# Kernel tuning notes

Hardware: AMD Instinct MI355X
Metric: run time of the kernel (lower is better)

## Reference

```python
import jax, jax.numpy as jnp
import numpy as np

ITER = 50
SMOOTH = 1e-05


def _max_pool(x, window):
    # x: [B, C, D, H, W]; 'same' max pool with stride 1, -inf padding
    # (matches torch F.max_pool3d semantics with symmetric padding).
    win = (1, 1) + window
    pads = [(0, 0), (0, 0)] + [((w - 1) // 2, (w - 1) // 2) for w in window]
    return jax.lax.reduce_window(x, -jnp.inf, jax.lax.max, win, (1,) * 5, pads)


def soft_erode(img):
    p1 = -_max_pool(-img, (3, 1, 1))
    p2 = -_max_pool(-img, (1, 3, 1))
    p3 = -_max_pool(-img, (1, 1, 3))
    return jnp.minimum(jnp.minimum(p1, p2), p3)


def soft_dilate(img):
    return _max_pool(img, (3, 3, 3))


def soft_open(img):
    return soft_dilate(soft_erode(img))


def soft_skel(img, n_iter):
    skel = jax.nn.relu(img - soft_open(img))

    def body(_, carry):
        img, skel = carry
        img = soft_erode(img)
        delta = jax.nn.relu(img - soft_open(img))
        skel = skel + jax.nn.relu(delta - skel * delta)
        return (img, skel)

    _, skel = jax.lax.fori_loop(0, n_iter, body, (img, skel))
    return skel


def setup_inputs() -> dict:
    key = jax.random.key(0)
    k1, k2 = jax.random.split(key)
    shape = (2, 2, 96, 192, 192)
    pred = jax.random.uniform(k1, shape, dtype=jnp.float32)
    target = jax.random.uniform(k2, shape, dtype=jnp.float32)
    return {"pred": pred, "target": target}


def reference(pred, target):
    pred_fg = pred[:, 1:2, ...]
    target_fg = target[:, 1:2, ...].astype(jnp.float32)
    skel_pred = soft_skel(pred_fg, ITER)
    skel_target = soft_skel(target_fg, ITER)
    tprec = (jnp.sum(skel_pred * target_fg) + SMOOTH) / (jnp.sum(skel_pred) + SMOOTH)
    tsens = (jnp.sum(skel_target * pred_fg) + SMOOTH) / (jnp.sum(skel_target) + SMOOTH)
    cl_dice = 2.0 * (tprec * tsens) / (tprec + tsens + SMOOTH)
    return 1.0 - cl_dice
```

## Files before the change

kernel.cpp:

```cpp
#include <hip/hip_runtime.h>
#include <math.h>

#define NX 192
#define NY 192
#define NZ 96
#define NV 4
#define VOL (NZ * NY * NX)
#define NTOT (NV * VOL)
#define YS NX
#define ZS (NY * NX)

#define TX 48
#define TYB 24
#define NG 14
#define R2A 30
#define RROW 28
#define ZCHM 12
#define NCH 8

#define SLOT4(x) (((x) + 100) % 4)
#define SLOT3(x) (((x) + 99) % 3)
#define SLOT2(x) (((x) + 100) % 2)

#define HINF  0x7C00u
#define HNINF 0xFC00u

typedef _Float16 h2v __attribute__((ext_vector_type(2)));

struct __align__(8) H4u { unsigned lo, hi; };

__device__ __forceinline__ h2v h2_of(unsigned u) { return __builtin_bit_cast(h2v, u); }
__device__ __forceinline__ unsigned u_of(h2v h) { return __builtin_bit_cast(unsigned, h); }

__device__ __forceinline__ void ldsbar() {
    asm volatile("s_waitcnt lgkmcnt(0)" ::: "memory");
    __builtin_amdgcn_s_barrier();
}

__device__ __forceinline__ H4u h4min(H4u a, H4u b) {
    H4u r;
    r.lo = u_of(__builtin_elementwise_min(h2_of(a.lo), h2_of(b.lo)));
    r.hi = u_of(__builtin_elementwise_min(h2_of(a.hi), h2_of(b.hi)));
    return r;
}
__device__ __forceinline__ H4u h4max(H4u a, H4u b) {
    H4u r;
    r.lo = u_of(__builtin_elementwise_max(h2_of(a.lo), h2_of(b.lo)));
    r.hi = u_of(__builtin_elementwise_max(h2_of(a.hi), h2_of(b.hi)));
    return r;
}
__device__ __forceinline__ H4u h4add(H4u a, H4u b) {
    H4u r;
    r.lo = u_of(h2_of(a.lo) + h2_of(b.lo));
    r.hi = u_of(h2_of(a.hi) + h2_of(b.hi));
    return r;
}
__device__ __forceinline__ H4u h4sub(H4u a, H4u b) {
    H4u r;
    r.lo = u_of(h2_of(a.lo) - h2_of(b.lo));
    r.hi = u_of(h2_of(a.hi) - h2_of(b.hi));
    return r;
}
__device__ __forceinline__ H4u h4mul(H4u a, H4u b) {
    H4u r;
    r.lo = u_of(h2_of(a.lo) * h2_of(b.lo));
    r.hi = u_of(h2_of(a.hi) * h2_of(b.hi));
    return r;
}
__device__ __forceinline__ H4u h4skel(H4u s, H4u a, H4u dil) {
    const H4u HZ4 = { 0u, 0u };
    const H4u HONE = { 0x3C003C00u, 0x3C003C00u };
    H4u dd = h4max(h4sub(a, dil), HZ4);
    H4u t = h4mul(dd, h4sub(HONE, s));
    return h4add(s, h4max(t, HZ4));
}
__device__ __forceinline__ H4u shl1(H4u c, unsigned p16) {
    H4u r;
    r.lo = (c.lo << 16) | (p16 & 0xFFFFu);
    r.hi = (c.hi << 16) | (c.lo >> 16);
    return r;
}
__device__ __forceinline__ H4u shr1(H4u c, unsigned n16) {
    H4u r;
    r.lo = (c.lo >> 16) | (c.hi << 16);
    r.hi = (c.hi >> 16) | ((n16 & 0xFFFFu) << 16);
    return r;
}
__device__ __forceinline__ H4u f4_to_h4(float4 f) {
    h2v a, b;
    a[0] = (_Float16)f.x; a[1] = (_Float16)f.y;
    b[0] = (_Float16)f.z; b[1] = (_Float16)f.w;
    H4u r; r.lo = u_of(a); r.hi = u_of(b); return r;
}
__device__ __forceinline__ float4 h4_to_f4(H4u h) {
    h2v a = h2_of(h.lo), b = h2_of(h.hi);
    return make_float4((float)a[0], (float)a[1], (float)b[0], (float)b[1]);
}

template<bool FIRST>
__global__ __launch_bounds__(512, 8) void fused2_kernel(
    const float* __restrict__ pred, const float* __restrict__ target,
    const _Float16* __restrict__ Ain, _Float16* __restrict__ Eout,
    _Float16* __restrict__ skel)
{
    __shared__ H4u As[4][R2A][NG];
    __shared__ H4u E1c[3][RROW][NG];
    __shared__ H4u ZM1[2][RROW][NG];
    __shared__ H4u ZM2[2][RROW][NG];

    const int tid = threadIdx.x;
    const int lr  = tid >> 4;
    const int c   = tid & 15;
    const int cc  = (c < 14) ? c : 13;
    const int lre = (lr < RROW) ? lr : (RROW - 1);
    const int sr  = tid / 14;
    const int sg  = tid - sr * 14;

    const int x0 = blockIdx.x * TX;
    const int y0 = blockIdx.y * TYB;
    const int v  = blockIdx.z / NCH;
    const int ch = blockIdx.z % NCH;
    const int z0 = ch * ZCHM;
    const int z1 = z0 + ZCHM;

    const float* Af = nullptr;
    const _Float16* Ah = nullptr;
    if (FIRST) Af = ((v < 2) ? pred : target) + (size_t)((v & 1) * 2 + 1) * VOL;
    else       Ah = Ain + (size_t)v * VOL;
    _Float16* Ev = Eout + (size_t)v * VOL;
    _Float16* Sv = skel + (size_t)v * VOL;

    const H4u HP4 = { 0x7C007C00u, 0x7C007C00u };
    const H4u HN4 = { 0xFC00FC00u, 0xFC00FC00u };
    const H4u HZ4 = { 0u, 0u };

    const bool xlo = (x0 == 0);
    const bool xhi = (x0 + TX == NX);

    const int  gys  = y0 - 3 + sr;
    const int  gxs  = x0 - 4 + 4 * sg;
    const bool stIn = (sr < R2A) && (gys >= 0) && (gys < NY) &&
                      (gxs >= 0) && (gxs < NX);

    const int  gx   = x0 - 4 + 4 * c;
    const bool gxin = (c < 14) && (gx >= 0) && (gx < NX);
    const int  gyo  = y0 - 2 + lre;
    const bool yIn  = (gyo >= 0) && (gyo < NY);
    const bool uAct = (lr >= 2 && lr <= 25 && c >= 1 && c <= 12);
    const int  rdn  = (lre > 0) ? lre - 1 : 0;
    const int  rup  = (lre < RROW - 1) ? lre + 1 : (RROW - 1);

    auto stageLoad = [&](int za) -> H4u {
        H4u val = HP4;
        if (stIn && za >= 0 && za < NZ) {
            if (FIRST)
                val = f4_to_h4(*(const float4*)(Af + (size_t)za * ZS + gys * YS + gxs));
            else
                val = *(const H4u*)(Ah + (size_t)za * ZS + gys * YS + gxs);
        }
        return val;
    };
    auto stageWrite = [&](int za, H4u val) {
        if (sr < R2A) As[SLOT4(za)][sr][sg] = val;
    };

    auto e1compute = [&](int zp, H4u& cenOut) -> H4u {
        if (zp >= NZ) { cenOut = HP4; return HP4; }
        const int s_c = SLOT4(zp), s_m = SLOT4(zp - 1), s_p = SLOT4(zp + 1);
        const bool hp = (zp + 1 < NZ);
        const int ar = lre + 1;
        H4u cen = As[s_c][ar][cc];
        H4u ylo = As[s_c][ar - 1][cc];
        H4u yhi = As[s_c][ar + 1][cc];
        H4u zlo = As[s_m][ar][cc];
        H4u zhi = hp ? As[s_p][ar][cc] : HP4;
        cenOut = cen;
        unsigned lw = __shfl_up(cen.hi, 1) >> 16;
        unsigned rx = __shfl_down(cen.lo, 1) & 0xFFFFu;
        if (c == 0) lw = HINF;
        H4u m = h4min(cen, shl1(cen, lw));
        m = h4min(m, shr1(cen, rx));
        m = h4min(m, h4min(ylo, yhi));
        m = h4min(m, h4min(zlo, zhi));
        if (zp < 0 || !yIn || !gxin) m = HP4;
        if (lr < RROW && c < 14) E1c[SLOT3(zp)][lr][c] = m;
        return m;
    };

    stageWrite(z0 - 3, stageLoad(z0 - 3));
    stageWrite(z0 - 2, stageLoad(z0 - 2));
    stageWrite(z0 - 1, stageLoad(z0 - 1));
    stageWrite(z0,     stageLoad(z0));
    ldsbar();
    H4u aT, a1, a2 = HP4;
    H4u e1m2 = e1compute(z0 - 2, aT);
    H4u e1m1 = e1compute(z0 - 1, aT);
    ldsbar();
    stageWrite(z0 + 1, stageLoad(z0 + 1));
    ldsbar();
    H4u e1c = e1compute(z0, a1);
    stageWrite(z0 + 2, stageLoad(z0 + 2));
    ldsbar();

    H4u e1m3 = HP4;
    H4u e2c = HN4, e2m1 = HN4;
    H4u zm1_prev = HN4, zm2_prev = HN4;
    H4u skA = HZ4, sq1 = HZ4, sq2 = HZ4;

    for (int z = z0; z <= z1 + 2; ++z) {
        const bool doStage = (z <= z1 - 1);
        H4u stv = doStage ? stageLoad(z + 3) : HP4;
        H4u skN = HZ4;
        if (!FIRST && z < z1 && uAct)
            skN = *(const H4u*)(Sv + (size_t)z * ZS + gyo * YS + gx);

        H4u aC = HP4;
        H4u e1new = (z <= z1) ? e1compute(z + 1, aC) : HP4;

        H4u zm1w;
        {
            H4u t0 = (z >= 1) ? e1m1 : HN4;
            H4u t2 = (z + 1 < NZ) ? e1new : HN4;
            zm1w = h4max(t0, h4max(e1c, t2));
            if (!yIn || !gxin) zm1w = HN4;
            if (lr < RROW && c < 14) ZM1[SLOT2(z)][lr][c] = zm1w;
        }

        const int p = z - 1;
        H4u e2new = HN4;
        if (p >= 0 && p <= z1 && p < NZ) {
            H4u cen = e1m1;
            H4u zlo = e1m2;
            H4u zhi = e1c;
            H4u ylo = E1c[SLOT3(p)][rdn][cc];
            H4u yhi = E1c[SLOT3(p)][rup][cc];
            unsigned lwE = __shfl_up(cen.hi, 1) >> 16;
            unsigned rxE = __shfl_down(cen.lo, 1) & 0xFFFFu;
            if (c == 0) lwE = HINF;
            H4u m2 = h4min(cen, shl1(cen, lwE));
            m2 = h4min(m2, shr1(cen, rxE));
            m2 = h4min(m2, h4min(ylo, yhi));
            m2 = h4min(m2, h4min(zlo, zhi));
            if (yIn && gxin) {
                e2new = m2;
                if (p >= z0 && p < z1 && lr >= 2 && lr <= 25 && c >= 1 && c <= 12)
                    *(H4u*)(Ev + (size_t)p * ZS + gyo * YS + gx) = m2;
            }
        }

        H4u zm2w = h4max(e2m1, h4max(e2c, e2new));
        if (lr < RROW && c < 14) ZM2[SLOT2(z - 2)][lr][c] = zm2w;

        H4u spnew = HZ4;
        if (p >= z0 && p < z1) {
            H4u vm = h4max(ZM1[SLOT2(p)][rdn][cc],
                     h4max(zm1_prev, ZM1[SLOT2(p)][rup][cc]));
            unsigned lw = __shfl_up(vm.hi, 1) >> 16;
            unsigned rx = __shfl_down(vm.lo, 1) & 0xFFFFu;
            if (xlo && c == 1)  lw = HNINF;
            if (xhi && c == 12) rx = HNINF;
            if (uAct) {
                H4u dilh = h4max(h4max(shl1(vm, lw), vm), shr1(vm, rx));
                spnew = h4skel(skA, a2, dilh);
            }
        }

        const int q = z - 3;
        if (q >= z0 && q < z1) {
            H4u vm2 = h4max(ZM2[SLOT2(q)][rdn][cc],
                      h4max(zm2_prev, ZM2[SLOT2(q)][rup][cc]));
            unsigned lw = __shfl_up(vm2.hi, 1) >> 16;
            unsigned rx = __shfl_down(vm2.lo, 1) & 0xFFFFu;
            if (xlo && c == 1)  lw = HNINF;
            if (xhi && c == 12) rx = HNINF;
            if (uAct) {
                H4u dilh = h4max(h4max(shl1(vm2, lw), vm2), shr1(vm2, rx));
                H4u s = h4skel(sq2, e1m3, dilh);
                *(H4u*)(Sv + (size_t)q * ZS + gyo * YS + gx) = s;
            }
        }

        if (doStage) stageWrite(z + 3, stv);

        ldsbar();
        e1m3 = e1m2; e1m2 = e1m1; e1m1 = e1c; e1c = e1new;
        e2m1 = e2c; e2c = e2new;
        zm1_prev = zm1w; zm2_prev = zm2w;
        a2 = a1; a1 = aC;
        sq2 = sq1; sq1 = spnew; skA = skN;
    }
}

__global__ __launch_bounds__(512, 8) void last_kernel(
    const _Float16* __restrict__ Ain,
    const float* __restrict__ pred, const float* __restrict__ target,
    const _Float16* __restrict__ skel, double* __restrict__ sums)
{
    __shared__ H4u As[4][R2A][NG];
    __shared__ H4u ZM1[2][RROW][NG];
    __shared__ double sred[16];

    const int tid = threadIdx.x;
    const int lr  = tid >> 4;
    const int c   = tid & 15;
    const int cc  = (c < 14) ? c : 13;
    const int lre = (lr < RROW) ? lr : (RROW - 1);
    const int sr  = tid / 14;
    const int sg  = tid - sr * 14;

    const int x0 = blockIdx.x * TX;
    const int y0 = blockIdx.y * TYB;
    const int v  = blockIdx.z / NCH;
    const int ch = blockIdx.z % NCH;
    const int z0 = ch * ZCHM;
    const int z1 = z0 + ZCHM;

    const _Float16* Ah = Ain + (size_t)v * VOL;
    const _Float16* Sv = skel + (size_t)v * VOL;
    const float* Ov = ((v < 2) ? target : pred) + (size_t)((v & 1) * 2 + 1) * VOL;

    const H4u HP4 = { 0x7C007C00u, 0x7C007C00u };
    const H4u HN4 = { 0xFC00FC00u, 0xFC00FC00u };
    const H4u HZ4 = { 0u, 0u };
    const float4 ZERO4 = make_float4(0.f, 0.f, 0.f, 0.f);

    const bool xlo = (x0 == 0);
    const bool xhi = (x0 + TX == NX);

    const int  gys  = y0 - 3 + sr;
    const int  gxs  = x0 - 4 + 4 * sg;
    const bool stIn = (sr < R2A) && (gys >= 0) && (gys < NY) &&
                      (gxs >= 0) && (gxs < NX);

    const int  gx   = x0 - 4 + 4 * c;
    const bool gxin = (c < 14) && (gx >= 0) && (gx < NX);
    const int  gyo  = y0 - 2 + lre;
    const bool yIn  = (gyo >= 0) && (gyo < NY);
    const bool uAct = (lr >= 2 && lr <= 25 && c >= 1 && c <= 12);
    const int  rdn  = (lre > 0) ? lre - 1 : 0;
    const int  rup  = (lre < RROW - 1) ? lre + 1 : (RROW - 1);

    auto stageLoad = [&](int za) -> H4u {
        H4u val = HP4;
        if (stIn && za >= 0 && za < NZ)
            val = *(const H4u*)(Ah + (size_t)za * ZS + gys * YS + gxs);
        return val;
    };
    auto stageWrite = [&](int za, H4u val) {
        if (sr < R2A) As[SLOT4(za)][sr][sg] = val;
    };

    auto e1compute = [&](int zp, H4u& cenOut) -> H4u {
        if (zp >= NZ) { cenOut = HP4; return HP4; }
        const int s_c = SLOT4(zp), s_m = SLOT4(zp - 1), s_p = SLOT4(zp + 1);
        const bool hp = (zp + 1 < NZ);
        const int ar = lre + 1;
        H4u cen = As[s_c][ar][cc];
        H4u ylo = As[s_c][ar - 1][cc];
        H4u yhi = As[s_c][ar + 1][cc];
        H4u zlo = As[s_m][ar][cc];
        H4u zhi = hp ? As[s_p][ar][cc] : HP4;
        cenOut = cen;
        unsigned lw = __shfl_up(cen.hi, 1) >> 16;
        unsigned rx = __shfl_down(cen.lo, 1) & 0xFFFFu;
        if (c == 0) lw = HINF;
        H4u m = h4min(cen, shl1(cen, lw));
        m = h4min(m, shr1(cen, rx));
        m = h4min(m, h4min(ylo, yhi));
        m = h4min(m, h4min(zlo, zhi));
        if (zp < 0 || !yIn || !gxin) m = HP4;
        return m;
    };

    stageWrite(z0 - 2, stageLoad(z0 - 2));
    stageWrite(z0 - 1, stageLoad(z0 - 1));
    stageWrite(z0,     stageLoad(z0));
    stageWrite(z0 + 1, stageLoad(z0 + 1));
    ldsbar();
    H4u aT, a1, a2 = HP4;
    H4u e1m1 = e1compute(z0 - 1, aT);
    H4u e1c  = e1compute(z0, a1);
    ldsbar();
    stageWrite(z0 + 2, stageLoad(z0 + 2));
    ldsbar();

    H4u zmP = HN4;
    H4u skA = HZ4;
    float4 oA = ZERO4;
    double afd = 0.0, afs = 0.0;

    for (int z = z0; z <= z1; ++z) {
        const bool doStage = (z <= z1 - 2);
        H4u stv = doStage ? stageLoad(z + 3) : HP4;
        H4u skN = HZ4;
        float4 oN = ZERO4;
        if (z < z1 && uAct) {
            skN = *(const H4u*)(Sv + (size_t)z * ZS + gyo * YS + gx);
            oN  = *(const float4*)(Ov + (size_t)z * ZS + gyo * YS + gx);
        }

        H4u aC = HP4;
        H4u e1new = (z + 1 <= z1) ? e1compute(z + 1, aC) : HP4;

        H4u zm1w = HN4;
        if (z <= z1 - 1) {
            H4u t0 = (z >= 1) ? e1m1 : HN4;
            H4u t2 = (z + 1 < NZ) ? e1new : HN4;
            zm1w = h4max(t0, h4max(e1c, t2));
            if (!yIn || !gxin) zm1w = HN4;
            if (lr < RROW && c < 14) ZM1[SLOT2(z)][lr][c] = zm1w;
        }

        const int p = z - 1;
        if (p >= z0 && p < z1) {
            H4u vm = h4max(ZM1[SLOT2(p)][rdn][cc],
                     h4max(zmP, ZM1[SLOT2(p)][rup][cc]));
            unsigned lw = __shfl_up(vm.hi, 1) >> 16;
            unsigned rx = __shfl_down(vm.lo, 1) & 0xFFFFu;
            if (xlo && c == 1)  lw = HNINF;
            if (xhi && c == 12) rx = HNINF;
            if (uAct) {
                H4u dilh = h4max(h4max(shl1(vm, lw), vm), shr1(vm, rx));
                H4u s = h4skel(skA, a2, dilh);
                float4 sf = h4_to_f4(s);
                afd += (double)(sf.x * oA.x + sf.y * oA.y +
                                sf.z * oA.z + sf.w * oA.w);
                afs += (double)(sf.x + sf.y + sf.z + sf.w);
            }
        }

        if (doStage) stageWrite(z + 3, stv);

        ldsbar();
        e1m1 = e1c; e1c = e1new;
        a2 = a1; a1 = aC;
        zmP = zm1w;
        skA = skN; oA = oN;
    }

#pragma unroll
    for (int off = 32; off > 0; off >>= 1) {
        afd += __shfl_down(afd, off, 64);
        afs += __shfl_down(afs, off, 64);
    }
    int lane = tid & 63, wid = tid >> 6;
    if (lane == 0) { sred[wid * 2] = afd; sred[wid * 2 + 1] = afs; }
    __syncthreads();
    if (tid == 0) {
        double fd = 0.0, fs = 0.0;
#pragma unroll
        for (int w = 0; w < 8; ++w) { fd += sred[w * 2]; fs += sred[w * 2 + 1]; }
        if (v < 2) { atomicAdd(&sums[0], fd); atomicAdd(&sums[1], fs); }
        else       { atomicAdd(&sums[2], fd); atomicAdd(&sums[3], fs); }
    }
}

__global__ void final_kernel(const double* __restrict__ sums,
                             float* __restrict__ out) {
    if (threadIdx.x == 0 && blockIdx.x == 0) {
        const double SM = 1e-5;
        double tprec = (sums[0] + SM) / (sums[1] + SM);
        double tsens = (sums[2] + SM) / (sums[3] + SM);
        double cl = 2.0 * tprec * tsens / (tprec + tsens + SM);
        out[0] = (float)(1.0 - cl);
    }
}

extern "C" void kernel_launch(void* const* d_in, const int* in_sizes, int n_in,
                              void* d_out, int out_size, void* d_ws, size_t ws_size,
                              hipStream_t stream) {
    const float* pred = (const float*)d_in[0];
    const float* target = (const float*)d_in[1];
    float* out = (float*)d_out;

    _Float16* H0 = (_Float16*)d_ws;
    _Float16* H1 = H0 + NTOT;
    _Float16* skel = H1 + NTOT;
    double* sums = (double*)(skel + NTOT);

    hipMemsetAsync(sums, 0, 4 * sizeof(double), stream);

    dim3 g(NX / TX, NY / TYB, NV * NCH);

    fused2_kernel<true><<<g, 512, 0, stream>>>(pred, target, H0, H0, skel);
    _Float16* A = H0;
    _Float16* B = H1;
    for (int j = 0; j < 24; ++j) {
        fused2_kernel<false><<<g, 512, 0, stream>>>(pred, target, A, B, skel);
        _Float16* t = A; A = B; B = t;
    }
    last_kernel<<<g, 512, 0, stream>>>(A, pred, target, skel, sums);

    final_kernel<<<1, 64, 0, stream>>>(sums, out);
}
```

Baseline: 1.427 ms.

## Fuse three erosion iterations per kernel launch with deeper z-pipeline

Adds a fused3 kernel that chains three erode/open/skeleton-update steps in one pass. It uses larger halos (32-row staging, 30-row erode buffers) and longer z chunks (24 planes, 4 chunks per volume). The launch sequence becomes 16 fused3 launches plus one fused2 launch, instead of 25 fused2 launches. The aim is to cut global memory round trips and launch count per iteration. The cost is more halo recomputation, more LDS use, and lower occupancy (launch bounds 512,2 and fewer blocks in z).

Result: slower. 1.479 ms (+3.7%).

```diff
diff --git a/kernel.cpp b/kernel.cpp
--- a/kernel.cpp
+++ b/kernel.cpp
@@ -13,10 +13,16 @@
 #define TX 48
 #define TYB 24
 #define NG 14
+
 #define R2A 30
 #define RROW 28
 #define ZCHM 12
 #define NCH 8
+
+#define A3R 32
+#define E3R 30
+#define Z3CH 24
+#define N3CH 4
 
 #define SLOT4(x) (((x) + 100) % 4)
 #define SLOT3(x) (((x) + 99) % 3)
@@ -95,6 +101,252 @@
 __device__ __forceinline__ float4 h4_to_f4(H4u h) {
     h2v a = h2_of(h.lo), b = h2_of(h.hi);
     return make_float4((float)a[0], (float)a[1], (float)b[0], (float)b[1]);
+}
+
+template<bool FIRST>
+__global__ __launch_bounds__(512, 2) void fused3_kernel(
+    const float* __restrict__ pred, const float* __restrict__ target,
+    const _Float16* __restrict__ Ain, _Float16* __restrict__ Eout,
+    _Float16* __restrict__ skel)
+{
+    __shared__ H4u As[4][A3R][NG];
+    __shared__ H4u E1c[3][E3R][NG];
+    __shared__ H4u E2c[3][E3R][NG];
+    __shared__ H4u ZM1[2][E3R][NG];
+    __shared__ H4u ZM2[2][E3R][NG];
+    __shared__ H4u ZM3[2][E3R][NG];
+
+    const int tid = threadIdx.x;
+    const int lr  = tid >> 4;
+    const int c   = tid & 15;
+    const int cc  = (c < 14) ? c : 13;
+    const int lre = (lr < E3R) ? lr : (E3R - 1);
+    const int sr  = tid / 14;
+    const int sg  = tid - sr * 14;
+
+    const int x0 = blockIdx.x * TX;
+    const int y0 = blockIdx.y * TYB;
+    const int v  = blockIdx.z / N3CH;
+    const int ch = blockIdx.z % N3CH;
+    const int z0 = ch * Z3CH;
+    const int z1 = z0 + Z3CH;
+
+    const float* Af = nullptr;
+    const _Float16* Ah = nullptr;
+    if (FIRST) Af = ((v < 2) ? pred : target) + (size_t)((v & 1) * 2 + 1) * VOL;
+    else       Ah = Ain + (size_t)v * VOL;
+    _Float16* Ev = Eout + (size_t)v * VOL;
+    _Float16* Sv = skel + (size_t)v * VOL;
+
+    const H4u HP4 = { 0x7C007C00u, 0x7C007C00u };
+    const H4u HN4 = { 0xFC00FC00u, 0xFC00FC00u };
+    const H4u HZ4 = { 0u, 0u };
+
+    const bool xlo = (x0 == 0);
+    const bool xhi = (x0 + TX == NX);
+
+    const int  gys  = y0 - 4 + sr;
+    const int  gxs  = x0 - 4 + 4 * sg;
+    const bool stIn = (sr < A3R) && (gys >= 0) && (gys < NY) &&
+                      (gxs >= 0) && (gxs < NX);
+
+    const int  gx   = x0 - 4 + 4 * c;
+    const bool gxin = (c < 14) && (gx >= 0) && (gx < NX);
+    const int  gyo  = y0 - 3 + lre;
+    const bool yIn  = (gyo >= 0) && (gyo < NY);
+    const bool uAct = (lr >= 3 && lr <= 26 && c >= 1 && c <= 12);
+    const int  rdn  = (lre > 0) ? lre - 1 : 0;
+    const int  rup  = (lre < E3R - 1) ? lre + 1 : (E3R - 1);
+
+    auto stageLoad = [&](int za) -> H4u {
+        H4u val = HP4;
+        if (stIn && za >= 0 && za < NZ) {
+            if (FIRST)
+                val = f4_to_h4(*(const float4*)(Af + (size_t)za * ZS + gys * YS + gxs));
+            else
+                val = *(const H4u*)(Ah + (size_t)za * ZS + gys * YS + gxs);
+        }
+        return val;
+    };
+    auto stageWrite = [&](int za, H4u val) {
+        if (sr < A3R) As[SLOT4(za)][sr][sg] = val;
+    };
+
+    auto erodeStep = [&](H4u cen, H4u zlo, H4u zhi, H4u ylo, H4u yhi) -> H4u {
+        unsigned lw = __shfl_up(cen.hi, 1) >> 16;
+        unsigned rx = __shfl_down(cen.lo, 1) & 0xFFFFu;
+        if (c == 0) lw = HINF;
+        H4u m = h4min(cen, shl1(cen, lw));
+        m = h4min(m, shr1(cen, rx));
+        m = h4min(m, h4min(ylo, yhi));
+        return h4min(m, h4min(zlo, zhi));
+    };
+
+    auto e1compute = [&](int zp, H4u& cenOut) -> H4u {
+        if (zp >= NZ) { cenOut = HP4; return HP4; }
+        const int s_c = SLOT4(zp), s_m = SLOT4(zp - 1), s_p = SLOT4(zp + 1);
+        const bool hp = (zp + 1 < NZ);
+        const int ar = lre + 1;
+        H4u cen = As[s_c][ar][cc];
+        H4u ylo = As[s_c][ar - 1][cc];
+        H4u yhi = As[s_c][ar + 1][cc];
+        H4u zlo = As[s_m][ar][cc];
+        H4u zhi = hp ? As[s_p][ar][cc] : HP4;
+        cenOut = cen;
+        H4u m = erodeStep(cen, zlo, zhi, ylo, yhi);
+        if (zp < 0 || !yIn || !gxin) m = HP4;
+        if (lr < E3R && c < 14) E1c[SLOT3(zp)][lr][c] = m;
+        return m;
+    };
+
+    auto dilateX = [&](H4u vm) -> H4u {
+        unsigned lw = __shfl_up(vm.hi, 1) >> 16;
+        unsigned rx = __shfl_down(vm.lo, 1) & 0xFFFFu;
+        if (xlo && c == 1)  lw = HNINF;
+        if (xhi && c == 12) rx = HNINF;
+        return h4max(h4max(shl1(vm, lw), vm), shr1(vm, rx));
+    };
+
+    stageWrite(z0 - 6, stageLoad(z0 - 6));
+    stageWrite(z0 - 5, stageLoad(z0 - 5));
+    stageWrite(z0 - 4, stageLoad(z0 - 4));
+    stageWrite(z0 - 3, stageLoad(z0 - 3));
+    ldsbar();
+    H4u aX, aPa, aPb;
+    H4u e1_m5 = e1compute(z0 - 5, aX);
+    ldsbar();
+    stageWrite(z0 - 2, stageLoad(z0 - 2));
+    H4u e1_m4 = e1compute(z0 - 4, aX);
+    ldsbar();
+    stageWrite(z0 - 1, stageLoad(z0 - 1));
+    H4u e1_m3 = e1compute(z0 - 3, aX);
+    H4u e2_m4 = HN4;
+    if (z0 - 4 >= 0 && z0 - 4 < NZ) {
+        H4u m2 = erodeStep(e1_m4, e1_m5, e1_m3,
+                           E1c[SLOT3(z0 - 4)][rdn][cc], E1c[SLOT3(z0 - 4)][rup][cc]);
+        if (yIn && gxin) e2_m4 = m2;
+    }
+    ldsbar();
+    stageWrite(z0, stageLoad(z0));
+    H4u e1_m2 = e1compute(z0 - 2, aX);
+    H4u e2_m3 = HN4;
+    if (z0 - 3 >= 0 && z0 - 3 < NZ) {
+        H4u m2 = erodeStep(e1_m3, e1_m4, e1_m2,
+                           E1c[SLOT3(z0 - 3)][rdn][cc], E1c[SLOT3(z0 - 3)][rup][cc]);
+        H4u st = (yIn && gxin) ? m2 : HP4;
+        if (yIn && gxin) e2_m3 = m2;
+        if (lr < E3R && c < 14) E2c[SLOT3(z0 - 3)][lr][c] = st;
+    }
+    ldsbar();
+    stageWrite(z0 + 1, stageLoad(z0 + 1));
+    H4u e1_m1 = e1compute(z0 - 1, aPa);
+    H4u e2_m2 = HN4;
+    if (z0 - 2 >= 0 && z0 - 2 < NZ) {
+        H4u m2 = erodeStep(e1_m2, e1_m3, e1_m1,
+                           E1c[SLOT3(z0 - 2)][rdn][cc], E1c[SLOT3(z0 - 2)][rup][cc]);
+        H4u st = (yIn && gxin) ? m2 : HP4;
+        if (yIn && gxin) e2_m2 = m2;
+        if (lr < E3R && c < 14) E2c[SLOT3(z0 - 2)][lr][c] = st;
+    }
+    ldsbar();
+    stageWrite(z0 + 2, stageLoad(z0 + 2));
+    H4u e1_z0 = e1compute(z0, aPb);
+    ldsbar();
+
+    H4u e1m3 = e1_m3, e1m2 = e1_m2, e1m1 = e1_m1, e1c = e1_z0;
+    H4u e2c = e2_m2, e2m1 = e2_m3, e2m2 = e2_m4, e2m3 = HN4;
+    H4u e3m1 = HN4, e3m2 = HN4;
+    H4u zm1_prev = HN4, zm2_prev = HN4, zm3_prev = HN4;
+    H4u skA = HZ4, sq1 = HZ4, sq2 = HZ4, sr1 = HZ4, sr2 = HZ4;
+    H4u a1 = aPb, a2 = aPa;
+
+    for (int z = z0; z <= z1 + 4; ++z) {
+        const bool doStage = (z <= z1);
+        H4u stv = doStage ? stageLoad(z + 3) : HP4;
+        H4u skN = HZ4;
+        if (!FIRST && z < z1 && uAct)
+            skN = *(const H4u*)(Sv + (size_t)z * ZS + gyo * YS + gx);
+
+        H4u aC = HP4;
+        H4u e1new = (z + 1 <= z1 + 2) ? e1compute(z + 1, aC) : HP4;
+
+        H4u zm1w;
+        {
+            H4u t0 = (z >= 1) ? e1m1 : HN4;
+            H4u t2 = (z + 1 < NZ) ? e1new : HN4;
+            zm1w = h4max(t0, h4max(e1c, t2));
+            if (!yIn || !gxin) zm1w = HN4;
+            if (lr < E3R && c < 14) ZM1[SLOT2(z)][lr][c] = zm1w;
+        }
+
+        const int p = z - 1;
+        H4u e2new = HN4;
+        if (p >= 0 && p <= z1 + 1 && p < NZ) {
+            H4u m2 = erodeStep(e1m1, e1m2, e1c,
+                               E1c[SLOT3(p)][rdn][cc], E1c[SLOT3(p)][rup][cc]);
+            H4u st = (yIn && gxin) ? m2 : HP4;
+            if (yIn && gxin) e2new = m2;
+            if (lr < E3R && c < 14) E2c[SLOT3(p)][lr][c] = st;
+        }
+
+        H4u zm2w = h4max(e2m1, h4max(e2c, e2new));
+        if (lr < E3R && c < 14) ZM2[SLOT2(z - 2)][lr][c] = zm2w;
+
+        H4u spnew = HZ4;
+        if (p >= z0 && p < z1) {
+            H4u vm = h4max(ZM1[SLOT2(p)][rdn][cc],
+                     h4max(zm1_prev, ZM1[SLOT2(p)][rup][cc]));
+            H4u dil = dilateX(vm);
+            if (uAct) spnew = h4skel(skA, a2, dil);
+        }
+
+        const int e = z - 3;
+        H4u e3new = HN4;
+        if (e >= 0 && e <= z1 && e < NZ) {
+            H4u zloE = (e >= 1)      ? e2m2 : HP4;
+            H4u zhiE = (e + 1 < NZ)  ? e2c  : HP4;
+            H4u m3 = erodeStep(e2m1, zloE, zhiE,
+                               E2c[SLOT3(e)][rdn][cc], E2c[SLOT3(e)][rup][cc]);
+            if (yIn && gxin) {
+                e3new = m3;
+                if (e >= z0 && e < z1 && uAct)
+                    *(H4u*)(Ev + (size_t)e * ZS + gyo * YS + gx) = m3;
+            }
+        }
+
+        H4u zm3w = h4max(e3m2, h4max(e3m1, e3new));
+        if (lr < E3R && c < 14) ZM3[SLOT2(z - 4)][lr][c] = zm3w;
+
+        H4u srnew = HZ4;
+        if (e >= z0 && e < z1) {
+            H4u vm2 = h4max(ZM2[SLOT2(e)][rdn][cc],
+                      h4max(zm2_prev, ZM2[SLOT2(e)][rup][cc]));
+            H4u dil = dilateX(vm2);
+            if (uAct) srnew = h4skel(sq2, e1m3, dil);
+        }
+
+        const int q3 = z - 5;
+        if (q3 >= z0 && q3 < z1) {
+            H4u vm3 = h4max(ZM3[SLOT2(q3)][rdn][cc],
+                      h4max(zm3_prev, ZM3[SLOT2(q3)][rup][cc]));
+            H4u dil = dilateX(vm3);
+            if (uAct) {
+                H4u s = h4skel(sr2, e2m3, dil);
+                *(H4u*)(Sv + (size_t)q3 * ZS + gyo * YS + gx) = s;
+            }
+        }
+
+        if (doStage) stageWrite(z + 3, stv);
+
+        ldsbar();
+        e1m3 = e1m2; e1m2 = e1m1; e1m1 = e1c; e1c = e1new;
+        e2m3 = e2m2; e2m2 = e2m1; e2m1 = e2c; e2c = e2new;
+        e3m2 = e3m1; e3m1 = e3new;
+        zm1_prev = zm1w; zm2_prev = zm2w; zm3_prev = zm3w;
+        a2 = a1; a1 = aC;
+        sq2 = sq1; sq1 = spnew; sr2 = sr1; sr1 = srnew;
+        skA = skN;
+    }
 }
 
 template<bool FIRST>
@@ -104,7 +356,7 @@
     _Float16* __restrict__ skel)
 {
     __shared__ H4u As[4][R2A][NG];
-    __shared__ H4u E1c[3][RROW][NG];
+    __shared__ H4u E1s[3][RROW][NG];
     __shared__ H4u ZM1[2][RROW][NG];
     __shared__ H4u ZM2[2][RROW][NG];
 
@@ -183,7 +435,7 @@
         m = h4min(m, h4min(ylo, yhi));
         m = h4min(m, h4min(zlo, zhi));
         if (zp < 0 || !yIn || !gxin) m = HP4;
-        if (lr < RROW && c < 14) E1c[SLOT3(zp)][lr][c] = m;
+        if (lr < RROW && c < 14) E1s[SLOT3(zp)][lr][c] = m;
         return m;
     };
 
@@ -232,8 +484,8 @@
             H4u cen = e1m1;
             H4u zlo = e1m2;
             H4u zhi = e1c;
-            H4u ylo = E1c[SLOT3(p)][rdn][cc];
-            H4u yhi = E1c[SLOT3(p)][rup][cc];
+            H4u ylo = E1s[SLOT3(p)][rdn][cc];
+            H4u yhi = E1s[SLOT3(p)][rup][cc];
             unsigned lwE = __shfl_up(cen.hi, 1) >> 16;
             unsigned rxE = __shfl_down(cen.lo, 1) & 0xFFFFu;
             if (c == 0) lwE = HINF;
@@ -480,16 +732,19 @@
 
     hipMemsetAsync(sums, 0, 4 * sizeof(double), stream);
 
-    dim3 g(NX / TX, NY / TYB, NV * NCH);
-
-    fused2_kernel<true><<<g, 512, 0, stream>>>(pred, target, H0, H0, skel);
+    dim3 g3(NX / TX, NY / TYB, NV * N3CH);
+    dim3 g2(NX / TX, NY / TYB, NV * NCH);
+
+    fused3_kernel<true><<<g3, 512, 0, stream>>>(pred, target, H0, H0, skel);
     _Float16* A = H0;
     _Float16* B = H1;
-    for (int j = 0; j < 24; ++j) {
-        fused2_kernel<false><<<g, 512, 0, stream>>>(pred, target, A, B, skel);
+    for (int j = 0; j < 15; ++j) {
+        fused3_kernel<false><<<g3, 512, 0, stream>>>(pred, target, A, B, skel);
         _Float16* t = A; A = B; B = t;
     }
-    last_kernel<<<g, 512, 0, stream>>>(A, pred, target, skel, sums);
+    fused2_kernel<false><<<g2, 512, 0, stream>>>(pred, target, A, B, skel);
+    _Float16* t = A; A = B; B = t;
+    last_kernel<<<g2, 512, 0, stream>>>(A, pred, target, skel, sums);
 
     final_kernel<<<1, 64, 0, stream>>>(sums, out);
 }
```
